# Kernel optimization log

Measured on AMD Instinct MI355X. Metric: run time of the kernel, lower is better.

Reference implementation:

```python
import jax, jax.numpy as jnp
import numpy as np

N_EXPERT_CAPACITY = 2  # init kwarg; k = S * capacity // E


def setup_inputs() -> dict:
    key = jax.random.key(0)
    k1, k2, k3, k4 = jax.random.split(key, 4)
    B, S, D, E, F = 8, 1024, 1024, 8, 2048
    # kaiming-uniform-ish scales
    x = jax.random.normal(k1, (B, S, D), dtype=jnp.float32)
    choice_w = jax.random.uniform(k2, (E, D), dtype=jnp.float32, minval=-1.0, maxval=1.0) * (1.0 / np.sqrt(D))
    w1 = jax.random.uniform(k3, (E, D, F), dtype=jnp.float32, minval=-1.0, maxval=1.0) * (1.0 / np.sqrt(D))
    w2 = jax.random.uniform(k4, (E, F, D), dtype=jnp.float32, minval=-1.0, maxval=1.0) * (1.0 / np.sqrt(F))
    return {"x": x, "choice_w": choice_w, "w1": w1, "w2": w2}


def reference(x, choice_w, w1, w2):
    B, S, D = x.shape
    E = choice_w.shape[0]
    k = S * N_EXPERT_CAPACITY // E  # tokens per expert (expert-choice)
    # router softmax over experts: [B, S, E]
    probs = jax.nn.softmax(jnp.einsum('bsd,ed->bse', x, choice_w), axis=-1)
    # each expert picks its top-k tokens: G, I are [B, E, k]
    G, I = jax.lax.top_k(jnp.swapaxes(probs, -1, -2), k)
    # dispatch: gather tokens instead of one-hot matmul (same math)
    x_in = jnp.take_along_axis(x[:, None, :, :], I[..., None], axis=2)  # [B, E, k, D]
    # per-expert MLP with SiLU
    h = jax.nn.silu(jnp.einsum('bekd,edf->bekf', x_in, w1))  # [B, E, k, F]
    x_mlp = jnp.einsum('bekf,efd->bekd', h, w2)              # [B, E, k, D]
    # combine: weighted scatter-add back to token positions (equals P,G,x_mlp einsum)
    b_idx = jnp.arange(B)[:, None, None]  # [B,1,1] broadcasts with I [B,E,k]
    out = jnp.zeros_like(x).at[b_idx, I].add(G[..., None] * x_mlp)
    return out
```

## Files before the change

kernel.cpp:

```cpp
#include <hip/hip_runtime.h>
#include <hip/hip_bf16.h>
#include <math.h>

#define B_   8
#define S_   1024
#define D_   1024
#define E_   8
#define F_   2048
#define KCAP 256

typedef __bf16 bf16x8 __attribute__((ext_vector_type(8)));
typedef float  floatx4 __attribute__((ext_vector_type(4)));
typedef unsigned short ushortx8 __attribute__((ext_vector_type(8)));

__device__ __forceinline__ unsigned short f2b(float f) {
    union { float f; unsigned int u; } v; v.f = f;
    unsigned int u = v.u;
    u += 0x7fffu + ((u >> 16) & 1u);
    return (unsigned short)(u >> 16);
}
__device__ __forceinline__ float b2f(unsigned short u) {
    union { unsigned int u; float f; } v; v.u = ((unsigned)u) << 16; return v.f;
}

__device__ __forceinline__ void gl_lds16(const void* g, void* l) {
    __builtin_amdgcn_global_load_lds(
        (const __attribute__((address_space(1))) void*)g,
        (__attribute__((address_space(3))) void*)l, 16, 0, 0);
}

__device__ __forceinline__ unsigned long long topk_key(float p, int s) {
    return (((unsigned long long)__float_as_uint(p)) << 10) | (unsigned)(S_ - 1 - s);
}

__global__ void router_kernel(const float* __restrict__ x, const float* __restrict__ cw,
                              float* __restrict__ probs, unsigned short* __restrict__ xb) {
    int gid  = blockIdx.x * 256 + threadIdx.x;
    int wave = gid >> 6;
    int lane = gid & 63;
    int b = wave >> 10;
    int s = wave & (S_ - 1);
    const float* xrow = x + ((size_t)b * S_ + s) * D_;
    unsigned short* xbrow = xb + ((size_t)b * S_ + s) * D_;
    float acc[E_];
#pragma unroll
    for (int e = 0; e < E_; e++) acc[e] = 0.f;
#pragma unroll
    for (int it = 0; it < D_ / 256; it++) {
        int i = it * 256 + lane * 4;
        float4 xv = *(const float4*)(xrow + i);
        ushort4 o;
        o.x = f2b(xv.x); o.y = f2b(xv.y); o.z = f2b(xv.z); o.w = f2b(xv.w);
        *(ushort4*)(xbrow + i) = o;
#pragma unroll
        for (int e = 0; e < E_; e++) {
            float4 wv = *(const float4*)(cw + e * D_ + i);
            acc[e] = fmaf(xv.x, wv.x, fmaf(xv.y, wv.y, fmaf(xv.z, wv.z, fmaf(xv.w, wv.w, acc[e]))));
        }
    }
#pragma unroll
    for (int e = 0; e < E_; e++) {
        float v = acc[e];
#pragma unroll
        for (int off = 32; off >= 1; off >>= 1) v += __shfl_down(v, off, 64);
        acc[e] = v;
    }
    if (lane == 0) {
        float m = acc[0];
#pragma unroll
        for (int e = 1; e < E_; e++) m = fmaxf(m, acc[e]);
        float sum = 0.f;
#pragma unroll
        for (int e = 0; e < E_; e++) { acc[e] = __expf(acc[e] - m); sum += acc[e]; }
        float inv = 1.f / sum;
#pragma unroll
        for (int e = 0; e < E_; e++) probs[((size_t)b * E_ + e) * S_ + s] = acc[e] * inv;
    }
}

__global__ void topk_rank_kernel(const float* __restrict__ probs, int* __restrict__ R4) {
    int g  = blockIdx.x;
    int be = g >> 2, c = g & 3;
    int tid = threadIdx.x;
    const float* rowp = probs + (size_t)be * S_;
    __shared__ unsigned long long kc[256];
    {
        int t = c * 256 + tid;
        kc[tid] = topk_key(rowp[t], t);
    }
    unsigned long long k[4];
    int r[4] = {0, 0, 0, 0};
#pragma unroll
    for (int q = 0; q < 4; q++) k[q] = topk_key(rowp[q * 256 + tid], q * 256 + tid);
    __syncthreads();
#pragma unroll 8
    for (int t = 0; t < 256; t++) {
        unsigned long long kt = kc[t];
#pragma unroll
        for (int q = 0; q < 4; q++) r[q] += (kt > k[q]);
    }
    int* Rb = R4 + (g << 10);
#pragma unroll
    for (int q = 0; q < 4; q++) Rb[q * 256 + tid] = r[q];
}

__global__ void topk_finalize_kernel(const float* __restrict__ probs, const int* __restrict__ R4,
                                     int* __restrict__ I, float* __restrict__ G,
                                     unsigned short* __restrict__ Pmap) {
    int be = blockIdx.x;
    int b = be >> 3, e = be & 7;
    int tid = threadIdx.x;
    for (int i = tid; i < S_; i += 256)
        Pmap[((size_t)(b * S_ + i)) * E_ + e] = 0;
    __syncthreads();
    const float* rowp = probs + (size_t)be * S_;
    const int* Rb = R4 + (be << 12);
#pragma unroll
    for (int q = 0; q < 4; q++) {
        int s = q * 256 + tid;
        int rank = Rb[s] + Rb[1024 + s] + Rb[2048 + s] + Rb[3072 + s];
        if (rank < KCAP) {
            I[be * KCAP + rank] = s;
            G[be * KCAP + rank] = rowp[s];
            Pmap[((size_t)(b * S_ + s)) * E_ + e] = (unsigned short)(rank + 1);
        }
    }
}

__global__ void transpose_cvt_kernel(const float* __restrict__ in, unsigned short* __restrict__ out,
                                     int R, int C) {
    __shared__ float tile[32][33];
    int e = blockIdx.z;
    int c0 = blockIdx.x * 32, r0 = blockIdx.y * 32;
    const float* ine = in + (size_t)e * R * C;
    unsigned short* oute = out + (size_t)e * R * C;
    int tid = threadIdx.x;
    int row = tid >> 3, cs = tid & 7;
    float4 v = *(const float4*)(ine + (size_t)(r0 + row) * C + c0 + cs * 4);
    tile[row][cs * 4 + 0] = v.x; tile[row][cs * 4 + 1] = v.y;
    tile[row][cs * 4 + 2] = v.z; tile[row][cs * 4 + 3] = v.w;
    __syncthreads();
    int c = tid >> 3, rq = tid & 7;
    ushort4 o;
    o.x = f2b(tile[rq * 4 + 0][c]); o.y = f2b(tile[rq * 4 + 1][c]);
    o.z = f2b(tile[rq * 4 + 2][c]); o.w = f2b(tile[rq * 4 + 3][c]);
    *(ushort4*)(oute + (size_t)(c0 + c) * R + r0 + rq * 4) = o;
}


__global__ __launch_bounds__(256, 4) void gemm1_kernel(
    const unsigned short* __restrict__ xb,
    const unsigned short* __restrict__ w1t,
    const int* __restrict__ I,
    unsigned short* __restrict__ H)
{
    const int g  = blockIdx.x;
    const int e  = g & 7;
    const int rr = g >> 3;
    const int b  = rr >> 5;
    const int t5 = rr & 31;
    const int be = b * 8 + e;
    const int mt = t5 & 1;
    const int nt = t5 >> 1;
    const int tid = threadIdx.x;

    __shared__ __align__(16) unsigned short Asm[128 * 64];
    __shared__ __align__(16) unsigned short Bsm[128 * 64];
    __shared__ unsigned int ArowS[128];

    if (tid < 128) {
        int tok = I[(size_t)be * KCAP + mt * 128 + tid];
        ArowS[tid] = (unsigned)((b * S_ + tok) * D_);
    }
    __syncthreads();

    const int r8   = tid >> 3;
    const int kseg = (tid & 7) ^ (r8 & 7);
    unsigned aoffW[4];
#pragma unroll
    for (int w = 0; w < 4; w++) aoffW[w] = ArowS[w * 32 + r8] + kseg * 8;
    const size_t boff0 = ((size_t)e * F_ + nt * 128 + r8) * D_ + kseg * 8;

    const int lane = tid & 63;
    const int wv   = tid >> 6;
    const int wm   = (wv & 1) * 64;
    const int wn   = (wv >> 1) * 64;
    const int l15  = lane & 15;
    const int quad = lane >> 4;
    const int x0   = (quad ^ (l15 & 7)) * 8;

    int aoffs[4], boffs[4];
#pragma unroll
    for (int i = 0; i < 4; i++) {
        aoffs[i] = (wm + i * 16 + l15) * 64 + x0;
        boffs[i] = (wn + i * 16 + l15) * 64 + x0;
    }

    floatx4 acc[4][4];
#pragma unroll
    for (int i = 0; i < 4; i++)
#pragma unroll
        for (int j = 0; j < 4; j++) acc[i][j] = (floatx4){0.f, 0.f, 0.f, 0.f};

    for (int k0 = 0; k0 < D_; k0 += 64) {
#pragma unroll
        for (int w = 0; w < 4; w++) {
            gl_lds16(xb  + aoffW[w] + k0,                    &Asm[(w * 256 + tid) * 8]);
            gl_lds16(w1t + boff0 + (size_t)w * 32 * D_ + k0, &Bsm[(w * 256 + tid) * 8]);
        }
        __syncthreads();
        bf16x8 af[4], bfr[4];
#pragma unroll
        for (int i = 0; i < 4; i++) {
            af[i]  = *(const bf16x8*)&Asm[aoffs[i]];
            bfr[i] = *(const bf16x8*)&Bsm[boffs[i]];
        }
#pragma unroll
        for (int i = 0; i < 4; i++)
#pragma unroll
            for (int j = 0; j < 4; j++)
                acc[i][j] = __builtin_amdgcn_mfma_f32_16x16x32_bf16(af[i], bfr[j], acc[i][j], 0, 0, 0);
#pragma unroll
        for (int i = 0; i < 4; i++) {
            af[i]  = *(const bf16x8*)&Asm[aoffs[i] ^ 32];
            bfr[i] = *(const bf16x8*)&Bsm[boffs[i] ^ 32];
        }
#pragma unroll
        for (int i = 0; i < 4; i++)
#pragma unroll
            for (int j = 0; j < 4; j++)
                acc[i][j] = __builtin_amdgcn_mfma_f32_16x16x32_bf16(af[i], bfr[j], acc[i][j], 0, 0, 0);
        __syncthreads();
    }

    unsigned short* Hbe = H + (size_t)be * KCAP * F_;
#pragma unroll
    for (int i = 0; i < 4; i++) {
#pragma unroll
        for (int r = 0; r < 4; r++) {
            int m = mt * 128 + wm + i * 16 + quad * 4 + r;
            unsigned short* hrow = Hbe + (size_t)m * F_ + nt * 128;
#pragma unroll
            for (int j = 0; j < 4; j++) {
                float v = acc[i][j][r];
                float sv = v / (1.f + __expf(-v));
                hrow[wn + j * 16 + l15] = f2b(sv);
            }
        }
    }
}

__global__ __launch_bounds__(256, 4) void gemm2_kernel(
    const unsigned short* __restrict__ H,
    const unsigned short* __restrict__ w2t,
    unsigned short* __restrict__ xmlp)
{
    const int g  = blockIdx.x;
    const int e  = g & 7;
    const int rr = g >> 3;
    const int b  = rr >> 4;
    const int t4 = rr & 15;
    const int be = b * 8 + e;
    const int mt = t4 & 1;
    const int nt = t4 >> 1;
    const int tid = threadIdx.x;

    __shared__ __align__(16) unsigned short Asm[128 * 64];
    __shared__ __align__(16) unsigned short Bsm[128 * 64];

    const int r8   = tid >> 3;
    const int kseg = (tid & 7) ^ (r8 & 7);
    const size_t aoff0 = ((size_t)be * KCAP + mt * 128 + r8) * F_ + kseg * 8;
    const size_t boff0 = ((size_t)e * D_ + nt * 128 + r8) * F_ + kseg * 8;

    const int lane = tid & 63;
    const int wv   = tid >> 6;
    const int wm   = (wv & 1) * 64;
    const int wn   = (wv >> 1) * 64;
    const int l15  = lane & 15;
    const int quad = lane >> 4;
    const int x0   = (quad ^ (l15 & 7)) * 8;

    int aoffs[4], boffs[4];
#pragma unroll
    for (int i = 0; i < 4; i++) {
        aoffs[i] = (wm + i * 16 + l15) * 64 + x0;
        boffs[i] = (wn + i * 16 + l15) * 64 + x0;
    }

    floatx4 acc[4][4];
#pragma unroll
    for (int i = 0; i < 4; i++)
#pragma unroll
        for (int j = 0; j < 4; j++) acc[i][j] = (floatx4){0.f, 0.f, 0.f, 0.f};

    for (int k0 = 0; k0 < F_; k0 += 64) {
#pragma unroll
        for (int w = 0; w < 4; w++) {
            gl_lds16(H   + aoff0 + (size_t)w * 32 * F_ + k0, &Asm[(w * 256 + tid) * 8]);
            gl_lds16(w2t + boff0 + (size_t)w * 32 * F_ + k0, &Bsm[(w * 256 + tid) * 8]);
        }
        __syncthreads();
        bf16x8 af[4], bfr[4];
#pragma unroll
        for (int i = 0; i < 4; i++) {
            af[i]  = *(const bf16x8*)&Asm[aoffs[i]];
            bfr[i] = *(const bf16x8*)&Bsm[boffs[i]];
        }
#pragma unroll
        for (int i = 0; i < 4; i++)
#pragma unroll
            for (int j = 0; j < 4; j++)
                acc[i][j] = __builtin_amdgcn_mfma_f32_16x16x32_bf16(af[i], bfr[j], acc[i][j], 0, 0, 0);
#pragma unroll
        for (int i = 0; i < 4; i++) {
            af[i]  = *(const bf16x8*)&Asm[aoffs[i] ^ 32];
            bfr[i] = *(const bf16x8*)&Bsm[boffs[i] ^ 32];
        }
#pragma unroll
        for (int i = 0; i < 4; i++)
#pragma unroll
            for (int j = 0; j < 4; j++)
                acc[i][j] = __builtin_amdgcn_mfma_f32_16x16x32_bf16(af[i], bfr[j], acc[i][j], 0, 0, 0);
        __syncthreads();
    }

    unsigned short* Xbe = xmlp + (size_t)be * KCAP * D_;
#pragma unroll
    for (int i = 0; i < 4; i++) {
#pragma unroll
        for (int r = 0; r < 4; r++) {
            int m = mt * 128 + wm + i * 16 + quad * 4 + r;
            unsigned short* orow = Xbe + (size_t)m * D_ + nt * 128;
#pragma unroll
            for (int j = 0; j < 4; j++)
                orow[wn + j * 16 + l15] = f2b(acc[i][j][r]);
        }
    }
}

__global__ void combine_kernel(const unsigned short* __restrict__ xmlp,
                               const unsigned short* __restrict__ Pmap,
                               const float* __restrict__ G,
                               float* __restrict__ out) {
    int gid  = blockIdx.x * 256 + threadIdx.x;
    int wave = gid >> 6;
    int lane = gid & 63;
    int b = wave >> 10;
    float acc[16];
#pragma unroll
    for (int i = 0; i < 16; i++) acc[i] = 0.f;
    const unsigned short* pm = Pmap + (size_t)wave * E_;
#pragma unroll
    for (int e = 0; e < E_; e++) {
        int pe = pm[e];
        if (pe) {
            int beslot = (b * E_ + e) * KCAP + (pe - 1);
            float g = G[beslot];
            const unsigned short* rw = xmlp + (size_t)beslot * D_ + lane * 16;
            ushortx8 r0 = *(const ushortx8*)(rw);
            ushortx8 r1 = *(const ushortx8*)(rw + 8);
#pragma unroll
            for (int i = 0; i < 8; i++) {
                acc[i]     = fmaf(g, b2f(r0[i]), acc[i]);
                acc[8 + i] = fmaf(g, b2f(r1[i]), acc[8 + i]);
            }
        }
    }
    float* orow = out + (size_t)wave * D_ + lane * 16;
    ((float4*)orow)[0] = make_float4(acc[0],  acc[1],  acc[2],  acc[3]);
    ((float4*)orow)[1] = make_float4(acc[4],  acc[5],  acc[6],  acc[7]);
    ((float4*)orow)[2] = make_float4(acc[8],  acc[9],  acc[10], acc[11]);
    ((float4*)orow)[3] = make_float4(acc[12], acc[13], acc[14], acc[15]);
}

extern "C" void kernel_launch(void* const* d_in, const int* in_sizes, int n_in,
                              void* d_out, int out_size, void* d_ws, size_t ws_size,
                              hipStream_t stream) {
    const float* x  = (const float*)d_in[0];
    const float* cw = (const float*)d_in[1];
    const float* w1 = (const float*)d_in[2];
    const float* w2 = (const float*)d_in[3];
    float* out = (float*)d_out;

    char* ws = (char*)d_ws;
    float*          probs = (float*)(ws);
    int*            Ibuf  = (int*)(ws + 262144);
    float*          Gbuf  = (float*)(ws + 327680);
    unsigned short* Pmap  = (unsigned short*)(ws + 393216);
    unsigned short* xb    = (unsigned short*)(ws + 524288);
    unsigned short* wT    = (unsigned short*)(ws + 17301504);
    unsigned short* Hbuf  = (unsigned short*)(ws + 50855936);
    unsigned short* xmlp  = (unsigned short*)(ws + 117964800);
    int*            R4    = (int*)xmlp;

    router_kernel<<<(B_ * S_ * 64) / 256, 256, 0, stream>>>(x, cw, probs, xb);
    topk_rank_kernel<<<B_ * E_ * 4, 256, 0, stream>>>(probs, R4);
    topk_finalize_kernel<<<B_ * E_, 256, 0, stream>>>(probs, R4, Ibuf, Gbuf, Pmap);
    transpose_cvt_kernel<<<dim3(F_ / 32, D_ / 32, E_), 256, 0, stream>>>(w1, wT, D_, F_);
    gemm1_kernel<<<B_ * E_ * 2 * (F_ / 128), 256, 0, stream>>>(xb, wT, Ibuf, Hbuf);
    transpose_cvt_kernel<<<dim3(D_ / 32, F_ / 32, E_), 256, 0, stream>>>(w2, wT, F_, D_);
    gemm2_kernel<<<B_ * E_ * 2 * (D_ / 128), 256, 0, stream>>>(Hbuf, wT, xmlp);
    combine_kernel<<<(B_ * S_ * 64) / 256, 256, 0, stream>>>(xmlp, Pmap, Gbuf, out);
}
```

Measured before the change: 366.1 us.

## Fuse router with weight transposes, and fold combine into gemm2 via atomics

Merges the router, output zeroing and both weight transpose/convert passes into a single prep kernel, with larger 64x64 transpose tiles. The gemm2 epilogue now scales by the gate weight and atomically adds straight into the output rows picked by the token indices. This removes the Pmap, the bf16 xmlp intermediate and the separate combine kernel, along with their memory traffic and launches. In exchange it adds fp32 atomic contention and makes the summation order nondeterministic.

```diff
diff --git a/kernel.cpp b/kernel.cpp
--- a/kernel.cpp
+++ b/kernel.cpp
@@ -11,7 +11,6 @@
 
 typedef __bf16 bf16x8 __attribute__((ext_vector_type(8)));
 typedef float  floatx4 __attribute__((ext_vector_type(4)));
-typedef unsigned short ushortx8 __attribute__((ext_vector_type(8)));
 
 __device__ __forceinline__ unsigned short f2b(float f) {
     union { float f; unsigned int u; } v; v.f = f;
@@ -19,9 +18,6 @@
     u += 0x7fffu + ((u >> 16) & 1u);
     return (unsigned short)(u >> 16);
 }
-__device__ __forceinline__ float b2f(unsigned short u) {
-    union { unsigned int u; float f; } v; v.u = ((unsigned)u) << 16; return v.f;
-}
 
 __device__ __forceinline__ void gl_lds16(const void* g, void* l) {
     __builtin_amdgcn_global_load_lds(
@@ -33,48 +29,98 @@
     return (((unsigned long long)__float_as_uint(p)) << 10) | (unsigned)(S_ - 1 - s);
 }
 
-__global__ void router_kernel(const float* __restrict__ x, const float* __restrict__ cw,
-                              float* __restrict__ probs, unsigned short* __restrict__ xb) {
-    int gid  = blockIdx.x * 256 + threadIdx.x;
-    int wave = gid >> 6;
-    int lane = gid & 63;
-    int b = wave >> 10;
-    int s = wave & (S_ - 1);
-    const float* xrow = x + ((size_t)b * S_ + s) * D_;
-    unsigned short* xbrow = xb + ((size_t)b * S_ + s) * D_;
-    float acc[E_];
-#pragma unroll
-    for (int e = 0; e < E_; e++) acc[e] = 0.f;
-#pragma unroll
-    for (int it = 0; it < D_ / 256; it++) {
-        int i = it * 256 + lane * 4;
-        float4 xv = *(const float4*)(xrow + i);
+__device__ __forceinline__ void transpose64(const float* __restrict__ in, unsigned short* __restrict__ out,
+                                            int R, int C, int rt, int ct, int tid, float (*tile)[65]) {
+    int r0 = rt * 64, c0 = ct * 64;
+    int row = tid >> 2, q = tid & 3;
+    const float* src = in + (size_t)(r0 + row) * C + c0 + q * 16;
+    float4 v0 = ((const float4*)src)[0];
+    float4 v1 = ((const float4*)src)[1];
+    float4 v2 = ((const float4*)src)[2];
+    float4 v3 = ((const float4*)src)[3];
+    float* tr = &tile[row][q * 16];
+    tr[0]  = v0.x; tr[1]  = v0.y; tr[2]  = v0.z; tr[3]  = v0.w;
+    tr[4]  = v1.x; tr[5]  = v1.y; tr[6]  = v1.z; tr[7]  = v1.w;
+    tr[8]  = v2.x; tr[9]  = v2.y; tr[10] = v2.z; tr[11] = v2.w;
+    tr[12] = v3.x; tr[13] = v3.y; tr[14] = v3.z; tr[15] = v3.w;
+    __syncthreads();
+    int c = tid >> 2;
+    unsigned short* dst = out + (size_t)(c0 + c) * R + r0 + q * 16;
+#pragma unroll
+    for (int k4 = 0; k4 < 4; k4++) {
         ushort4 o;
-        o.x = f2b(xv.x); o.y = f2b(xv.y); o.z = f2b(xv.z); o.w = f2b(xv.w);
-        *(ushort4*)(xbrow + i) = o;
+        o.x = f2b(tile[q * 16 + k4 * 4 + 0][c]);
+        o.y = f2b(tile[q * 16 + k4 * 4 + 1][c]);
+        o.z = f2b(tile[q * 16 + k4 * 4 + 2][c]);
+        o.w = f2b(tile[q * 16 + k4 * 4 + 3][c]);
+        ((ushort4*)dst)[k4] = o;
+    }
+}
+
+__global__ __launch_bounds__(256) void prep_kernel(
+    const float* __restrict__ x, const float* __restrict__ cw,
+    const float* __restrict__ w1, const float* __restrict__ w2,
+    float* __restrict__ probs, unsigned short* __restrict__ xb,
+    unsigned short* __restrict__ w1t, unsigned short* __restrict__ w2t,
+    float* __restrict__ out) {
+    __shared__ float tile[64][65];
+    const int blk = blockIdx.x;
+    const int tid = threadIdx.x;
+    if (blk < 2048) {
+        float4 z = make_float4(0.f, 0.f, 0.f, 0.f);
+        float4* oz = (float4*)out + blk * 1024 + tid;
+        oz[0] = z; oz[256] = z; oz[512] = z; oz[768] = z;
+        int gid  = blk * 256 + tid;
+        int wave = gid >> 6;
+        int lane = gid & 63;
+        int b = wave >> 10;
+        int s = wave & (S_ - 1);
+        const float* xrow = x + ((size_t)b * S_ + s) * D_;
+        unsigned short* xbrow = xb + ((size_t)b * S_ + s) * D_;
+        float acc[E_];
+#pragma unroll
+        for (int e = 0; e < E_; e++) acc[e] = 0.f;
+#pragma unroll
+        for (int it = 0; it < D_ / 256; it++) {
+            int i = it * 256 + lane * 4;
+            float4 xv = *(const float4*)(xrow + i);
+            ushort4 o;
+            o.x = f2b(xv.x); o.y = f2b(xv.y); o.z = f2b(xv.z); o.w = f2b(xv.w);
+            *(ushort4*)(xbrow + i) = o;
+#pragma unroll
+            for (int e = 0; e < E_; e++) {
+                float4 wv = *(const float4*)(cw + e * D_ + i);
+                acc[e] = fmaf(xv.x, wv.x, fmaf(xv.y, wv.y, fmaf(xv.z, wv.z, fmaf(xv.w, wv.w, acc[e]))));
+            }
+        }
 #pragma unroll
         for (int e = 0; e < E_; e++) {
-            float4 wv = *(const float4*)(cw + e * D_ + i);
-            acc[e] = fmaf(xv.x, wv.x, fmaf(xv.y, wv.y, fmaf(xv.z, wv.z, fmaf(xv.w, wv.w, acc[e]))));
-        }
-    }
-#pragma unroll
-    for (int e = 0; e < E_; e++) {
-        float v = acc[e];
-#pragma unroll
-        for (int off = 32; off >= 1; off >>= 1) v += __shfl_down(v, off, 64);
-        acc[e] = v;
-    }
-    if (lane == 0) {
-        float m = acc[0];
-#pragma unroll
-        for (int e = 1; e < E_; e++) m = fmaxf(m, acc[e]);
-        float sum = 0.f;
-#pragma unroll
-        for (int e = 0; e < E_; e++) { acc[e] = __expf(acc[e] - m); sum += acc[e]; }
-        float inv = 1.f / sum;
-#pragma unroll
-        for (int e = 0; e < E_; e++) probs[((size_t)b * E_ + e) * S_ + s] = acc[e] * inv;
+            float v = acc[e];
+#pragma unroll
+            for (int off = 32; off >= 1; off >>= 1) v += __shfl_down(v, off, 64);
+            acc[e] = v;
+        }
+        if (lane == 0) {
+            float m = acc[0];
+#pragma unroll
+            for (int e = 1; e < E_; e++) m = fmaxf(m, acc[e]);
+            float sum = 0.f;
+#pragma unroll
+            for (int e = 0; e < E_; e++) { acc[e] = __expf(acc[e] - m); sum += acc[e]; }
+            float inv = 1.f / sum;
+#pragma unroll
+            for (int e = 0; e < E_; e++) probs[((size_t)b * E_ + e) * S_ + s] = acc[e] * inv;
+        }
+    } else if (blk < 6144) {
+        int t = blk - 2048;
+        int e = t >> 9, rem = t & 511;
+        transpose64(w1 + (size_t)e * D_ * F_, w1t + (size_t)e * F_ * D_,
+                    D_, F_, rem >> 5, rem & 31, tid, tile);
+    } else {
+        int t = blk - 6144;
+        int e = t >> 9, rem = t & 511;
+        transpose64(w2 + (size_t)e * F_ * D_, w2t + (size_t)e * D_ * F_,
+                    F_, D_, rem >> 4, rem & 15, tid, tile);
     }
 }
 
@@ -105,14 +151,9 @@
 }
 
 __global__ void topk_finalize_kernel(const float* __restrict__ probs, const int* __restrict__ R4,
-                                     int* __restrict__ I, float* __restrict__ G,
-                                     unsigned short* __restrict__ Pmap) {
+                                     int* __restrict__ I, float* __restrict__ G) {
     int be = blockIdx.x;
-    int b = be >> 3, e = be & 7;
     int tid = threadIdx.x;
-    for (int i = tid; i < S_; i += 256)
-        Pmap[((size_t)(b * S_ + i)) * E_ + e] = 0;
-    __syncthreads();
     const float* rowp = probs + (size_t)be * S_;
     const int* Rb = R4 + (be << 12);
 #pragma unroll
@@ -122,29 +163,8 @@
         if (rank < KCAP) {
             I[be * KCAP + rank] = s;
             G[be * KCAP + rank] = rowp[s];
-            Pmap[((size_t)(b * S_ + s)) * E_ + e] = (unsigned short)(rank + 1);
-        }
-    }
-}
-
-__global__ void transpose_cvt_kernel(const float* __restrict__ in, unsigned short* __restrict__ out,
-                                     int R, int C) {
-    __shared__ float tile[32][33];
-    int e = blockIdx.z;
-    int c0 = blockIdx.x * 32, r0 = blockIdx.y * 32;
-    const float* ine = in + (size_t)e * R * C;
-    unsigned short* oute = out + (size_t)e * R * C;
-    int tid = threadIdx.x;
-    int row = tid >> 3, cs = tid & 7;
-    float4 v = *(const float4*)(ine + (size_t)(r0 + row) * C + c0 + cs * 4);
-    tile[row][cs * 4 + 0] = v.x; tile[row][cs * 4 + 1] = v.y;
-    tile[row][cs * 4 + 2] = v.z; tile[row][cs * 4 + 3] = v.w;
-    __syncthreads();
-    int c = tid >> 3, rq = tid & 7;
-    ushort4 o;
-    o.x = f2b(tile[rq * 4 + 0][c]); o.y = f2b(tile[rq * 4 + 1][c]);
-    o.z = f2b(tile[rq * 4 + 2][c]); o.w = f2b(tile[rq * 4 + 3][c]);
-    *(ushort4*)(oute + (size_t)(c0 + c) * R + r0 + rq * 4) = o;
+        }
+    }
 }
 
 
@@ -253,7 +273,9 @@
 __global__ __launch_bounds__(256, 4) void gemm2_kernel(
     const unsigned short* __restrict__ H,
     const unsigned short* __restrict__ w2t,
-    unsigned short* __restrict__ xmlp)
+    const int* __restrict__ I,
+    const float* __restrict__ G,
+    float* __restrict__ out)
 {
     const int g  = blockIdx.x;
     const int e  = g & 7;
@@ -267,6 +289,15 @@
 
     __shared__ __align__(16) unsigned short Asm[128 * 64];
     __shared__ __align__(16) unsigned short Bsm[128 * 64];
+    __shared__ unsigned int OrowS[128];
+    __shared__ float Gs[128];
+
+    if (tid < 128) {
+        int tok = I[(size_t)be * KCAP + mt * 128 + tid];
+        OrowS[tid] = (unsigned)((b * S_ + tok) * D_);
+        Gs[tid] = G[(size_t)be * KCAP + mt * 128 + tid];
+    }
+    __syncthreads();
 
     const int r8   = tid >> 3;
     const int kseg = (tid & 7) ^ (r8 & 7);
@@ -325,53 +356,18 @@
         __syncthreads();
     }
 
-    unsigned short* Xbe = xmlp + (size_t)be * KCAP * D_;
 #pragma unroll
     for (int i = 0; i < 4; i++) {
 #pragma unroll
         for (int r = 0; r < 4; r++) {
-            int m = mt * 128 + wm + i * 16 + quad * 4 + r;
-            unsigned short* orow = Xbe + (size_t)m * D_ + nt * 128;
-#pragma unroll
-            for (int j = 0; j < 4; j++)
-                orow[wn + j * 16 + l15] = f2b(acc[i][j][r]);
-        }
-    }
-}
-
-__global__ void combine_kernel(const unsigned short* __restrict__ xmlp,
-                               const unsigned short* __restrict__ Pmap,
-                               const float* __restrict__ G,
-                               float* __restrict__ out) {
-    int gid  = blockIdx.x * 256 + threadIdx.x;
-    int wave = gid >> 6;
-    int lane = gid & 63;
-    int b = wave >> 10;
-    float acc[16];
-#pragma unroll
-    for (int i = 0; i < 16; i++) acc[i] = 0.f;
-    const unsigned short* pm = Pmap + (size_t)wave * E_;
-#pragma unroll
-    for (int e = 0; e < E_; e++) {
-        int pe = pm[e];
-        if (pe) {
-            int beslot = (b * E_ + e) * KCAP + (pe - 1);
-            float g = G[beslot];
-            const unsigned short* rw = xmlp + (size_t)beslot * D_ + lane * 16;
-            ushortx8 r0 = *(const ushortx8*)(rw);
-            ushortx8 r1 = *(const ushortx8*)(rw + 8);
-#pragma unroll
-            for (int i = 0; i < 8; i++) {
-                acc[i]     = fmaf(g, b2f(r0[i]), acc[i]);
-                acc[8 + i] = fmaf(g, b2f(r1[i]), acc[8 + i]);
-            }
-        }
-    }
-    float* orow = out + (size_t)wave * D_ + lane * 16;
-    ((float4*)orow)[0] = make_float4(acc[0],  acc[1],  acc[2],  acc[3]);
-    ((float4*)orow)[1] = make_float4(acc[4],  acc[5],  acc[6],  acc[7]);
-    ((float4*)orow)[2] = make_float4(acc[8],  acc[9],  acc[10], acc[11]);
-    ((float4*)orow)[3] = make_float4(acc[12], acc[13], acc[14], acc[15]);
+            int m = wm + i * 16 + quad * 4 + r;
+            float gw = Gs[m];
+            float* orow = out + OrowS[m] + nt * 128;
+#pragma unroll
+            for (int j = 0; j < 4; j++)
+                atomicAdd(orow + wn + j * 16 + l15, gw * acc[i][j][r]);
+        }
+    }
 }
 
 extern "C" void kernel_launch(void* const* d_in, const int* in_sizes, int n_in,
@@ -387,19 +383,15 @@
     float*          probs = (float*)(ws);
     int*            Ibuf  = (int*)(ws + 262144);
     float*          Gbuf  = (float*)(ws + 327680);
-    unsigned short* Pmap  = (unsigned short*)(ws + 393216);
-    unsigned short* xb    = (unsigned short*)(ws + 524288);
-    unsigned short* wT    = (unsigned short*)(ws + 17301504);
-    unsigned short* Hbuf  = (unsigned short*)(ws + 50855936);
-    unsigned short* xmlp  = (unsigned short*)(ws + 117964800);
-    int*            R4    = (int*)xmlp;
-
-    router_kernel<<<(B_ * S_ * 64) / 256, 256, 0, stream>>>(x, cw, probs, xb);
-    topk_rank_kernel<<<B_ * E_ * 4, 256, 0, stream>>>(probs, R4);
-    topk_finalize_kernel<<<B_ * E_, 256, 0, stream>>>(probs, R4, Ibuf, Gbuf, Pmap);
-    transpose_cvt_kernel<<<dim3(F_ / 32, D_ / 32, E_), 256, 0, stream>>>(w1, wT, D_, F_);
-    gemm1_kernel<<<B_ * E_ * 2 * (F_ / 128), 256, 0, stream>>>(xb, wT, Ibuf, Hbuf);
-    transpose_cvt_kernel<<<dim3(D_ / 32, F_ / 32, E_), 256, 0, stream>>>(w2, wT, F_, D_);
-    gemm2_kernel<<<B_ * E_ * 2 * (D_ / 128), 256, 0, stream>>>(Hbuf, wT, xmlp);
-    combine_kernel<<<(B_ * S_ * 64) / 256, 256, 0, stream>>>(xmlp, Pmap, Gbuf, out);
-}
+    unsigned short* xb    = (unsigned short*)(ws + 393216);
+    unsigned short* w1t   = (unsigned short*)(ws + 17170432);
+    unsigned short* w2t   = (unsigned short*)(ws + 50724864);
+    unsigned short* Hbuf  = (unsigned short*)(ws + 84279296);
+    int*            R4    = (int*)Hbuf;
+
+    prep_kernel<<<10240, 256, 0, stream>>>(x, cw, w1, w2, probs, xb, w1t, w2t, out);
+    topk_rank_kernel<<<256, 256, 0, stream>>>(probs, R4);
+    topk_finalize_kernel<<<B_ * E_, 256, 0, stream>>>(probs, R4, Ibuf, Gbuf);
+    gemm1_kernel<<<B_ * E_ * 2 * (F_ / 128), 256, 0, stream>>>(xb, w1t, Ibuf, Hbuf);
+    gemm2_kernel<<<B_ * E_ * 2 * (D_ / 128), 256, 0, stream>>>(Hbuf, w2t, Ibuf, Gbuf, out);
+}
```

After: 390.7 us. 1.07x slower.
